# Kernel tuning notes

Hardware: AMD Instinct MI355X
Metric: run time of the kernel (lower is better)

Reference implementation:

```python
import jax, jax.numpy as jnp
import numpy as np

KERNEL_SIZE = 128
NEG_INF = -1e30


def setup_inputs() -> dict:
    key = jax.random.key(0)
    ks = jax.random.split(key, 5)
    B, S, D, H = 4, 4096, 512, 512
    x = jax.random.normal(ks[0], (B, S, D), dtype=jnp.float32)
    # torch nn.Linear weights: [out_features, in_features], y = x @ W.T + b
    Wq_w = jax.random.normal(ks[1], (H, D), dtype=jnp.float32) * (1.0 / np.sqrt(D))
    Wq_b = jax.random.normal(ks[2], (H,), dtype=jnp.float32) * 0.01
    Wk_w = jax.random.normal(ks[3], (H, D), dtype=jnp.float32) * (1.0 / np.sqrt(D))
    Wk_b = jax.random.normal(ks[4], (H,), dtype=jnp.float32) * 0.01
    return {"x": x, "Wq_w": Wq_w, "Wq_b": Wq_b, "Wk_w": Wk_w, "Wk_b": Wk_b}


def reference(x, Wq_w, Wq_b, Wk_w, Wk_b):
    # q, k: [B, S, H]
    q = jnp.einsum('bsd,hd->bsh', x, Wq_w) + Wq_b
    k = jnp.einsum('bsd,hd->bsh', x, Wk_w) + Wk_b
    # dense scores [B, S, S]
    scores = jnp.einsum('bih,bjh->bij', q, k)
    # band mask: True where i-kernel_size+1 <= j <= i+kernel_size-1
    idx = jnp.arange(x.shape[1])
    band = jnp.abs(idx[:, None] - idx[None, :]) < KERNEL_SIZE  # [S, S]
    scores = jnp.where(band[None, :, :], scores, NEG_INF)
    attn = jax.nn.softmax(scores, axis=2)
    # attend over raw x (no V projection in original module)
    return jnp.einsum('bij,bjd->bid', attn, x)
```

## Files before the change

### kernel.cpp

```cpp
#include <hip/hip_runtime.h>
#include <hip/hip_bf16.h>

#define S_LEN 4096
#define NEG_INF_F (-1e30f)

typedef __attribute__((ext_vector_type(4))) float f32x4;
typedef __attribute__((ext_vector_type(8))) short s16x8;
typedef unsigned short u16;

static __device__ __forceinline__ u16 f2bf(float f) {
    unsigned u = __builtin_bit_cast(unsigned, f);
    unsigned r = u + 0x7FFFu + ((u >> 16) & 1u);
    return (u16)(r >> 16);
}
static __device__ __forceinline__ float bf2f(u16 h) {
    unsigned u = ((unsigned)h) << 16;
    return __builtin_bit_cast(float, u);
}
static __device__ __forceinline__ void split4(const float4 v, ushort4& hi, ushort4& lo) {
    hi.x = f2bf(v.x); lo.x = f2bf(v.x - bf2f(hi.x));
    hi.y = f2bf(v.y); lo.y = f2bf(v.y - bf2f(hi.y));
    hi.z = f2bf(v.z); lo.z = f2bf(v.z - bf2f(hi.z));
    hi.w = f2bf(v.w); lo.w = f2bf(v.w - bf2f(hi.w));
}
static __device__ __forceinline__ void gl_lds16(const void* g, void* l) {
    __builtin_amdgcn_global_load_lds(
        (const __attribute__((address_space(1))) void*)g,
        (__attribute__((address_space(3))) void*)l, 16, 0, 0);
}
static __device__ __forceinline__ int swz64(int row, int col_u16) {
    return row * 64 + (col_u16 ^ ((row & 7) << 3));
}
static __device__ __forceinline__ int swz320(int row, int col_u16) {
    return row * 320 + (col_u16 ^ ((row & 7) << 3));
}
static __device__ __forceinline__ int xcd_swz512(int bid) {
    return (bid & 7) * 64 + (bid >> 3);
}

__global__ __launch_bounds__(256) void split_xt_kernel(
    const float* __restrict__ x, u16* __restrict__ xh, u16* __restrict__ xl,
    u16* __restrict__ xT) {
    const int bid = blockIdx.x;
    const int dt = bid & 7, st = (bid >> 3) & 63, b = bid >> 9;
    const int s0 = st * 64, d0 = dt * 64;
    __shared__ u16 T[64][72];
    const int tid = threadIdx.x;
    #pragma unroll
    for (int i = 0; i < 4; ++i) {
        int idx = i * 256 + tid;
        int r = idx >> 4, c4 = (idx & 15) * 4;
        float4 v = *(const float4*)(x + (size_t)(b * S_LEN + s0 + r) * 512 + d0 + c4);
        ushort4 hi, lo; split4(v, hi, lo);
        *(ushort4*)(xh + (size_t)(b * S_LEN + s0 + r) * 512 + d0 + c4) = hi;
        *(ushort4*)(xl + (size_t)(b * S_LEN + s0 + r) * 512 + d0 + c4) = lo;
        *(ushort4*)&T[r][c4] = hi;
    }
    __syncthreads();
    #pragma unroll
    for (int i = 0; i < 2; ++i) {
        int idx = i * 256 + tid;
        int dr = idx >> 3, sc = idx & 7;
        s16x8 v;
        #pragma unroll
        for (int t = 0; t < 8; ++t) v[t] = (short)T[sc * 8 + t][dr];
        *(s16x8*)&xT[(size_t)(b * 512 + d0 + dr) * S_LEN + s0 + sc * 8] = v;
    }
}

__global__ __launch_bounds__(256) void mt_kernel(
    const float* __restrict__ Wk, const float* __restrict__ Wq,
    u16* __restrict__ Mth, u16* __restrict__ Mtl) {
    const int bm = blockIdx.x & 7, bn = blockIdx.x >> 3;
    const int m0 = bm * 64, n0 = bn * 64;
    __shared__ __align__(16) u16 Ath[64 * 72], Atl[64 * 72];
    __shared__ __align__(16) u16 Bth[64 * 72], Btl[64 * 72];
    const int tid = threadIdx.x, lane = tid & 63, w = tid >> 6;
    const int frow = lane & 15, fk = (lane >> 4) * 8;
    f32x4 acc[4] = {};

    for (int h0 = 0; h0 < 512; h0 += 64) {
        #pragma unroll
        for (int i = 0; i < 4; ++i) {
            int idx = i * 256 + tid;
            int h = idx >> 4, c4 = (idx & 15) * 4;
            float4 a = *(const float4*)(Wk + (size_t)(h0 + h) * 512 + m0 + c4);
            ushort4 ahi, alo; split4(a, ahi, alo);
            Ath[(c4 + 0) * 72 + h] = ahi.x; Atl[(c4 + 0) * 72 + h] = alo.x;
            Ath[(c4 + 1) * 72 + h] = ahi.y; Atl[(c4 + 1) * 72 + h] = alo.y;
            Ath[(c4 + 2) * 72 + h] = ahi.z; Atl[(c4 + 2) * 72 + h] = alo.z;
            Ath[(c4 + 3) * 72 + h] = ahi.w; Atl[(c4 + 3) * 72 + h] = alo.w;
            float4 b = *(const float4*)(Wq + (size_t)(h0 + h) * 512 + n0 + c4);
            ushort4 bhi, blo; split4(b, bhi, blo);
            Bth[(c4 + 0) * 72 + h] = bhi.x; Btl[(c4 + 0) * 72 + h] = blo.x;
            Bth[(c4 + 1) * 72 + h] = bhi.y; Btl[(c4 + 1) * 72 + h] = blo.y;
            Bth[(c4 + 2) * 72 + h] = bhi.z; Btl[(c4 + 2) * 72 + h] = blo.z;
            Bth[(c4 + 3) * 72 + h] = bhi.w; Btl[(c4 + 3) * 72 + h] = blo.w;
        }
        __syncthreads();
        #pragma unroll
        for (int kk = 0; kk < 2; ++kk) {
            s16x8 aH = *(const s16x8*)&Ath[(w * 16 + frow) * 72 + kk * 32 + fk];
            s16x8 aL = *(const s16x8*)&Atl[(w * 16 + frow) * 72 + kk * 32 + fk];
            #pragma unroll
            for (int ni = 0; ni < 4; ++ni) {
                s16x8 bH = *(const s16x8*)&Bth[(ni * 16 + frow) * 72 + kk * 32 + fk];
                s16x8 bL = *(const s16x8*)&Btl[(ni * 16 + frow) * 72 + kk * 32 + fk];
                acc[ni] = __builtin_amdgcn_mfma_f32_16x16x32_bf16(aH, bH, acc[ni], 0, 0, 0);
                acc[ni] = __builtin_amdgcn_mfma_f32_16x16x32_bf16(aH, bL, acc[ni], 0, 0, 0);
                acc[ni] = __builtin_amdgcn_mfma_f32_16x16x32_bf16(aL, bH, acc[ni], 0, 0, 0);
            }
        }
        __syncthreads();
    }
    #pragma unroll
    for (int ni = 0; ni < 4; ++ni) {
        int d1 = n0 + ni * 16 + frow;
        #pragma unroll
        for (int e = 0; e < 4; ++e) {
            int d2 = m0 + w * 16 + (lane >> 4) * 4 + e;
            float v = acc[ni][e];
            u16 hi = f2bf(v);
            Mth[(size_t)d2 * 512 + d1] = hi;
            Mtl[(size_t)d2 * 512 + d1] = f2bf(v - bf2f(hi));
        }
    }
}

__global__ __launch_bounds__(256) void u_kernel(
    const float* __restrict__ Wk, const float* __restrict__ bq,
    float* __restrict__ u) {
    __shared__ float red[4][64];
    const int tid = threadIdx.x, c = tid & 63, hg = tid >> 6;
    const int d2 = blockIdx.x * 64 + c;
    float acc = 0.f;
    for (int h = hg; h < 512; h += 4) acc += Wk[(size_t)h * 512 + d2] * bq[h];
    red[hg][c] = acc;
    __syncthreads();
    if (hg == 0) u[d2] = red[0][c] + red[1][c] + red[2][c] + red[3][c];
}

__global__ __launch_bounds__(512) void z_kernel(
    const u16* __restrict__ xh, const u16* __restrict__ xl,
    const u16* __restrict__ Mth, const u16* __restrict__ Mtl,
    const float* __restrict__ u, u16* __restrict__ zh, u16* __restrict__ zl) {
    const int w_ = xcd_swz512((int)blockIdx.x);
    const int bm = w_ >> 2, bn = w_ & 3;
    const int m0 = bm * 128, n0 = bn * 128;
    __shared__ __align__(16) u16 Ah[128 * 64], Al[128 * 64];
    __shared__ __align__(16) u16 Bh[128 * 64], Bl[128 * 64];
    const int tid = threadIdx.x, lane = tid & 63, w = tid >> 6;
    const int rg = w >> 2, cg = w & 3;
    const int frow = lane & 15, fk = (lane >> 4) * 8;
    f32x4 acc[4][2] = {};

    for (int k0 = 0; k0 < 512; k0 += 64) {
        #pragma unroll
        for (int i = 0; i < 2; ++i) {
            int idx = i * 512 + tid;
            int r = idx >> 3, c = idx & 7;
            int sc = (c ^ (r & 7)) * 8;
            gl_lds16(xh + (size_t)(m0 + r) * 512 + k0 + sc, &Ah[idx * 8]);
            gl_lds16(xl + (size_t)(m0 + r) * 512 + k0 + sc, &Al[idx * 8]);
            gl_lds16(Mth + (size_t)(n0 + r) * 512 + k0 + sc, &Bh[idx * 8]);
            gl_lds16(Mtl + (size_t)(n0 + r) * 512 + k0 + sc, &Bl[idx * 8]);
        }
        __syncthreads();
        #pragma unroll
        for (int kk = 0; kk < 2; ++kk) {
            s16x8 aH[4], aL[4], bH[2], bL[2];
            #pragma unroll
            for (int mi = 0; mi < 4; ++mi) {
                int row = rg * 64 + mi * 16 + frow;
                aH[mi] = *(const s16x8*)&Ah[swz64(row, kk * 32 + fk)];
                aL[mi] = *(const s16x8*)&Al[swz64(row, kk * 32 + fk)];
            }
            #pragma unroll
            for (int ni = 0; ni < 2; ++ni) {
                int row = cg * 32 + ni * 16 + frow;
                bH[ni] = *(const s16x8*)&Bh[swz64(row, kk * 32 + fk)];
                bL[ni] = *(const s16x8*)&Bl[swz64(row, kk * 32 + fk)];
            }
            #pragma unroll
            for (int mi = 0; mi < 4; ++mi)
                #pragma unroll
                for (int ni = 0; ni < 2; ++ni) {
                    acc[mi][ni] = __builtin_amdgcn_mfma_f32_16x16x32_bf16(aH[mi], bH[ni], acc[mi][ni], 0, 0, 0);
                    acc[mi][ni] = __builtin_amdgcn_mfma_f32_16x16x32_bf16(aH[mi], bL[ni], acc[mi][ni], 0, 0, 0);
                    acc[mi][ni] = __builtin_amdgcn_mfma_f32_16x16x32_bf16(aL[mi], bH[ni], acc[mi][ni], 0, 0, 0);
                }
        }
        __syncthreads();
    }
    #pragma unroll
    for (int ni = 0; ni < 2; ++ni) {
        int col = n0 + cg * 32 + ni * 16 + frow;
        float uv = u[col];
        #pragma unroll
        for (int mi = 0; mi < 4; ++mi) {
            int rbase = m0 + rg * 64 + mi * 16 + (lane >> 4) * 4;
            #pragma unroll
            for (int e = 0; e < 4; ++e) {
                float v = acc[mi][ni][e] + uv;
                u16 hi = f2bf(v);
                zh[(size_t)(rbase + e) * 512 + col] = hi;
                zl[(size_t)(rbase + e) * 512 + col] = f2bf(v - bf2f(hi));
            }
        }
    }
}

__global__ __launch_bounds__(512, 4) void attn_kernel(
    const u16* __restrict__ zh, const u16* __restrict__ zl,
    const u16* __restrict__ xh, const u16* __restrict__ xl,
    const u16* __restrict__ xT, float* __restrict__ out) {
    const int w_ = xcd_swz512((int)blockIdx.x);
    const int b = w_ >> 7, it2 = w_ & 127;
    const int i0 = it2 * 32, j0 = i0 - 128;
    const int mrow0 = b * S_LEN + i0;

    __shared__ __align__(16) u16 smem[36864];
    u16* Kh = smem;
    u16* Kl = smem + 18432;
    u16* PL = smem;
    u16* VL = smem + 10240;
    __shared__ float sred_max[32 * 4], sred_sum[32 * 4];

    const int tid = threadIdx.x, lane = tid & 63, w = tid >> 6;
    const int g = w >> 2, q = w & 3;
    const int frow = lane & 15, fk = (lane >> 4) * 8;
    const int tstart = g + q * 4;
    const int nt = (q == 3) ? 5 : 4;
    const size_t qoff = (size_t)(mrow0 + g * 16 + frow) * 512;

    f32x4 acc[5] = {};

    for (int t = 0; t < 8; ++t) {
        const int k0 = t * 64;
        s16x8 aH0 = *(const s16x8*)(zh + qoff + k0 + fk);
        s16x8 aH1 = *(const s16x8*)(zh + qoff + k0 + 32 + fk);
        s16x8 aL0 = *(const s16x8*)(zl + qoff + k0 + fk);
        s16x8 aL1 = *(const s16x8*)(zl + qoff + k0 + 32 + fk);
        #pragma unroll
        for (int i = 0; i < 9; ++i) {
            int f = i * 512 + tid;
            int idx = (f < 2304) ? f : f - 2304;
            int r = idx >> 3, c = idx & 7;
            int sc = (c ^ (r & 7)) * 8;
            int j = min(max(j0 + r, 0), S_LEN - 1);
            if (f < 2304)
                gl_lds16(xh + (size_t)(b * S_LEN + j) * 512 + k0 + sc, &Kh[idx * 8]);
            else
                gl_lds16(xl + (size_t)(b * S_LEN + j) * 512 + k0 + sc, &Kl[idx * 8]);
        }
        __syncthreads();
        #pragma unroll
        for (int kk = 0; kk < 2; ++kk) {
            s16x8 aH = kk ? aH1 : aH0;
            s16x8 aL = kk ? aL1 : aL0;
            #pragma unroll
            for (int tt = 0; tt < 5; ++tt) {
                if (tt < nt) {
                    int krow = (tstart + tt) * 16 + frow;
                    s16x8 bH = *(const s16x8*)&Kh[swz64(krow, kk * 32 + fk)];
                    s16x8 bL = *(const s16x8*)&Kl[swz64(krow, kk * 32 + fk)];
                    acc[tt] = __builtin_amdgcn_mfma_f32_16x16x32_bf16(aH, bH, acc[tt], 0, 0, 0);
                    acc[tt] = __builtin_amdgcn_mfma_f32_16x16x32_bf16(aH, bL, acc[tt], 0, 0, 0);
                    acc[tt] = __builtin_amdgcn_mfma_f32_16x16x32_bf16(aL, bH, acc[tt], 0, 0, 0);
                }
            }
        }
        __syncthreads();
    }

    const int rq = (lane >> 4) * 4;
    #pragma unroll
    for (int e = 0; e < 4; ++e) {
        int r = g * 16 + rq + e;
        float m = NEG_INF_F;
        #pragma unroll
        for (int tt = 0; tt < 5; ++tt) {
            if (tt < nt) {
                int jj = (tstart + tt) * 16 + frow;
                int dj = jj - r, j = j0 + jj;
                if (dj >= 1 && dj <= 255 && j >= 0 && j < S_LEN) m = fmaxf(m, acc[tt][e]);
            }
        }
        #pragma unroll
        for (int d = 1; d < 16; d <<= 1) m = fmaxf(m, __shfl_xor(m, d));
        if (frow == 0) sred_max[r * 4 + q] = m;
    }
    __syncthreads();
    float sh[4];
    #pragma unroll
    for (int e = 0; e < 4; ++e) {
        int r = g * 16 + rq + e;
        float mx = fmaxf(fmaxf(sred_max[r * 4], sred_max[r * 4 + 1]),
                         fmaxf(sred_max[r * 4 + 2], sred_max[r * 4 + 3]));
        float s = 0.f;
        #pragma unroll
        for (int tt = 0; tt < 5; ++tt) {
            float pv = 0.f;
            if (tt < nt) {
                int jj = (tstart + tt) * 16 + frow;
                int dj = jj - r, j = j0 + jj;
                bool valid = (dj >= 1 && dj <= 255 && j >= 0 && j < S_LEN);
                pv = valid ? __expf(acc[tt][e] - mx) : 0.f;
            }
            acc[tt][e] = pv;
            s += pv;
        }
        #pragma unroll
        for (int d = 1; d < 16; d <<= 1) s += __shfl_xor(s, d);
        sh[e] = s;
    }
    if (frow == 0) {
        #pragma unroll
        for (int e = 0; e < 4; ++e) sred_sum[(g * 16 + rq + e) * 4 + q] = sh[e];
    }
    __syncthreads();
    float invv[4];
    #pragma unroll
    for (int e = 0; e < 4; ++e) {
        int r = g * 16 + rq + e;
        invv[e] = 1.f / (sred_sum[r * 4] + sred_sum[r * 4 + 1] +
                         sred_sum[r * 4 + 2] + sred_sum[r * 4 + 3]);
    }
    #pragma unroll
    for (int tt = 0; tt < 5; ++tt) {
        if (tt < nt) {
            int t = tstart + tt;
            #pragma unroll
            for (int e = 0; e < 4; ++e) {
                int r = g * 16 + rq + e;
                PL[swz320(r, t * 16 + frow)] = f2bf(acc[tt][e] * invv[e]);
            }
        }
    }
    if (q == 0) {
        int t = (g == 0) ? 17 : 0;
        int r = g * 16 + frow;
        #pragma unroll
        for (int e2 = 0; e2 < 4; ++e2)
            PL[swz320(r, t * 16 + (lane >> 4) * 4 + e2)] = 0;
    }

    for (int ds = 0; ds < 8; ++ds) {
        const int d0 = ds * 64;
        #pragma unroll
        for (int i = 0; i < 5; ++i) {
            int idx = i * 512 + tid;
            int dr = idx / 40, c8 = idx - dr * 40;
            int src = c8 ^ (dr & 7);
            int jb = j0 + src * 8;
            jb = min(max(jb, 0), S_LEN - 8);
            gl_lds16(xT + (size_t)(b * 512 + d0 + dr) * S_LEN + jb, &VL[idx * 8]);
        }
        __syncthreads();
        f32x4 po = {};
        #pragma unroll
        for (int jt = 0; jt < 9; ++jt) {
            s16x8 a = *(const s16x8*)&PL[swz320(g * 16 + frow, jt * 32 + fk)];
            s16x8 bv = *(const s16x8*)&VL[swz320(q * 16 + frow, jt * 32 + fk)];
            po = __builtin_amdgcn_mfma_f32_16x16x32_bf16(a, bv, po, 0, 0, 0);
        }
        #pragma unroll
        for (int e = 0; e < 4; ++e) {
            int r = mrow0 + g * 16 + rq + e;
            out[(size_t)r * 512 + d0 + q * 16 + frow] = po[e];
        }
        __syncthreads();
    }
}

extern "C" void kernel_launch(void* const* d_in, const int* in_sizes, int n_in,
                              void* d_out, int out_size, void* d_ws, size_t ws_size,
                              hipStream_t stream) {
    const float* x  = (const float*)d_in[0];
    const float* Wq = (const float*)d_in[1];
    const float* bq = (const float*)d_in[2];
    const float* Wk = (const float*)d_in[3];
    const float* bk = (const float*)d_in[4];
    (void)bk;
    float* out = (float*)d_out;

    u16* xh  = (u16*)d_ws;
    u16* xl  = xh + (size_t)8388608;
    u16* zh  = xl + (size_t)8388608;
    u16* zl  = zh + (size_t)8388608;
    u16* Mth = zl + (size_t)8388608;
    u16* Mtl = Mth + (size_t)262144;
    u16* xT  = Mtl + (size_t)262144;
    float* uv = (float*)(xT + (size_t)8388608);

    hipLaunchKernelGGL(split_xt_kernel, dim3(2048), dim3(256), 0, stream, x, xh, xl, xT);
    hipLaunchKernelGGL(mt_kernel, dim3(64), dim3(256), 0, stream, Wk, Wq, Mth, Mtl);
    hipLaunchKernelGGL(u_kernel, dim3(8), dim3(256), 0, stream, Wk, bq, uv);
    hipLaunchKernelGGL(z_kernel, dim3(512), dim3(512), 0, stream,
                       xh, xl, Mth, Mtl, uv, zh, zl);
    hipLaunchKernelGGL(attn_kernel, dim3(512), dim3(512), 0, stream,
                       zh, zl, xh, xl, xT, out);
}
```

Before: 141.2 us.

## Software-pipeline K and V tile loads through registers with prefetch

Replaces direct global-to-LDS async loads with register-staged prefetch: the next K/Q tile (and next V tile in the PV phase) is loaded into registers while MFMAs run on the current LDS tile, then written into swizzled LDS. It also raises wave priority around the MFMA blocks. The aim is to hide global-load latency behind compute. In exchange it adds register pressure from kreg/vreg plus extra barriers per iteration, which may lower occupancy.

```diff
diff --git a/kernel.cpp b/kernel.cpp
--- a/kernel.cpp
+++ b/kernel.cpp
@@ -235,29 +235,56 @@
 
     f32x4 acc[5] = {};
 
-    for (int t = 0; t < 8; ++t) {
+    s16x8 kreg[9];
+    auto kload = [&](int t) {
         const int k0 = t * 64;
-        s16x8 aH0 = *(const s16x8*)(zh + qoff + k0 + fk);
-        s16x8 aH1 = *(const s16x8*)(zh + qoff + k0 + 32 + fk);
-        s16x8 aL0 = *(const s16x8*)(zl + qoff + k0 + fk);
-        s16x8 aL1 = *(const s16x8*)(zl + qoff + k0 + 32 + fk);
         #pragma unroll
         for (int i = 0; i < 9; ++i) {
             int f = i * 512 + tid;
             int idx = (f < 2304) ? f : f - 2304;
             int r = idx >> 3, c = idx & 7;
-            int sc = (c ^ (r & 7)) * 8;
             int j = min(max(j0 + r, 0), S_LEN - 1);
-            if (f < 2304)
-                gl_lds16(xh + (size_t)(b * S_LEN + j) * 512 + k0 + sc, &Kh[idx * 8]);
-            else
-                gl_lds16(xl + (size_t)(b * S_LEN + j) * 512 + k0 + sc, &Kl[idx * 8]);
-        }
-        __syncthreads();
+            const u16* src = (f < 2304 ? xh : xl);
+            kreg[i] = *(const s16x8*)(src + (size_t)(b * S_LEN + j) * 512 + k0 + c * 8);
+        }
+    };
+    auto kwrite = [&]() {
+        #pragma unroll
+        for (int i = 0; i < 9; ++i) {
+            int f = i * 512 + tid;
+            int idx = (f < 2304) ? f : f - 2304;
+            int r = idx >> 3, c = idx & 7;
+            u16* dst = (f < 2304 ? Kh : Kl);
+            *(s16x8*)&dst[swz64(r, c * 8)] = kreg[i];
+        }
+    };
+
+    s16x8 zH0c, zH1c, zL0c, zL1c, zH0n, zH1n, zL0n, zL1n;
+    kload(0);
+    {
+        zH0c = *(const s16x8*)(zh + qoff + 0 + fk);
+        zH1c = *(const s16x8*)(zh + qoff + 32 + fk);
+        zL0c = *(const s16x8*)(zl + qoff + 0 + fk);
+        zL1c = *(const s16x8*)(zl + qoff + 32 + fk);
+    }
+
+    for (int t = 0; t < 8; ++t) {
+        __syncthreads();
+        kwrite();
+        __syncthreads();
+        if (t < 7) {
+            kload(t + 1);
+            const int k1 = (t + 1) * 64;
+            zH0n = *(const s16x8*)(zh + qoff + k1 + fk);
+            zH1n = *(const s16x8*)(zh + qoff + k1 + 32 + fk);
+            zL0n = *(const s16x8*)(zl + qoff + k1 + fk);
+            zL1n = *(const s16x8*)(zl + qoff + k1 + 32 + fk);
+        }
+        __builtin_amdgcn_s_setprio(1);
         #pragma unroll
         for (int kk = 0; kk < 2; ++kk) {
-            s16x8 aH = kk ? aH1 : aH0;
-            s16x8 aL = kk ? aL1 : aL0;
+            s16x8 aH = kk ? zH1c : zH0c;
+            s16x8 aL = kk ? zL1c : zL0c;
             #pragma unroll
             for (int tt = 0; tt < 5; ++tt) {
                 if (tt < nt) {
@@ -270,8 +297,31 @@
                 }
             }
         }
-        __syncthreads();
-    }
+        __builtin_amdgcn_s_setprio(0);
+        zH0c = zH0n; zH1c = zH1n; zL0c = zL0n; zL1c = zL1n;
+    }
+
+    s16x8 vreg[5];
+    auto vload = [&](int ds) {
+        const int d0 = ds * 64;
+        #pragma unroll
+        for (int i = 0; i < 5; ++i) {
+            int idx = i * 512 + tid;
+            int dr = idx / 40, c8 = idx - dr * 40;
+            int jb = j0 + c8 * 8;
+            jb = min(max(jb, 0), S_LEN - 8);
+            vreg[i] = *(const s16x8*)&xT[(size_t)(b * 512 + d0 + dr) * S_LEN + jb];
+        }
+    };
+    auto vwrite = [&]() {
+        #pragma unroll
+        for (int i = 0; i < 5; ++i) {
+            int idx = i * 512 + tid;
+            int dr = idx / 40, c8 = idx - dr * 40;
+            *(s16x8*)&VL[swz320(dr, c8 * 8)] = vreg[i];
+        }
+    };
+    vload(0);
 
     const int rq = (lane >> 4) * 4;
     #pragma unroll
@@ -346,30 +396,24 @@
     }
 
     for (int ds = 0; ds < 8; ++ds) {
-        const int d0 = ds * 64;
-        #pragma unroll
-        for (int i = 0; i < 5; ++i) {
-            int idx = i * 512 + tid;
-            int dr = idx / 40, c8 = idx - dr * 40;
-            int src = c8 ^ (dr & 7);
-            int jb = j0 + src * 8;
-            jb = min(max(jb, 0), S_LEN - 8);
-            gl_lds16(xT + (size_t)(b * 512 + d0 + dr) * S_LEN + jb, &VL[idx * 8]);
-        }
-        __syncthreads();
+        __syncthreads();
+        vwrite();
+        __syncthreads();
+        if (ds < 7) vload(ds + 1);
         f32x4 po = {};
+        __builtin_amdgcn_s_setprio(1);
         #pragma unroll
         for (int jt = 0; jt < 9; ++jt) {
             s16x8 a = *(const s16x8*)&PL[swz320(g * 16 + frow, jt * 32 + fk)];
             s16x8 bv = *(const s16x8*)&VL[swz320(q * 16 + frow, jt * 32 + fk)];
             po = __builtin_amdgcn_mfma_f32_16x16x32_bf16(a, bv, po, 0, 0, 0);
         }
+        __builtin_amdgcn_s_setprio(0);
         #pragma unroll
         for (int e = 0; e < 4; ++e) {
             int r = mrow0 + g * 16 + rq + e;
-            out[(size_t)r * 512 + d0 + q * 16 + frow] = po[e];
-        }
-        __syncthreads();
+            out[(size_t)r * 512 + ds * 64 + q * 16 + frow] = po[e];
+        }
     }
 }
 
```

Result: slower. 157.2 us (+11.3%).

## Load K and V MFMA operands directly from global memory, dropping LDS staging

Applied to the files above, without the earlier changes.

The attention kernel no longer stages key tiles and transposed-x value tiles through shared memory. Each wave now loads its MFMA B-operands straight from global memory into registers, which removes most __syncthreads barriers and shrinks LDS to just the probability tile. s_setprio is raised around the MFMA bursts. In exchange, rows shared between waves are fetched redundantly from global/L2, loads are less coalesced, and register pressure rises, which could hurt occupancy.

```diff
diff --git a/kernel.cpp b/kernel.cpp
--- a/kernel.cpp
+++ b/kernel.cpp
@@ -219,11 +219,7 @@
     const int i0 = it2 * 32, j0 = i0 - 128;
     const int mrow0 = b * S_LEN + i0;
 
-    __shared__ __align__(16) u16 smem[36864];
-    u16* Kh = smem;
-    u16* Kl = smem + 18432;
-    u16* PL = smem;
-    u16* VL = smem + 10240;
+    __shared__ __align__(16) u16 PL[32 * 320];
     __shared__ float sred_max[32 * 4], sred_sum[32 * 4];
 
     const int tid = threadIdx.x, lane = tid & 63, w = tid >> 6;
@@ -232,48 +228,50 @@
     const int tstart = g + q * 4;
     const int nt = (q == 3) ? 5 : 4;
     const size_t qoff = (size_t)(mrow0 + g * 16 + frow) * 512;
+    const int rq = (lane >> 4) * 4;
+
+    size_t rowoffs[5];
+    #pragma unroll
+    for (int tt = 0; tt < 5; ++tt) {
+        int krow = (tstart + tt) * 16 + frow;
+        int j = min(max(j0 + krow, 0), S_LEN - 1);
+        rowoffs[tt] = (size_t)(b * S_LEN + j) * 512;
+    }
 
     f32x4 acc[5] = {};
 
     for (int t = 0; t < 8; ++t) {
         const int k0 = t * 64;
-        s16x8 aH0 = *(const s16x8*)(zh + qoff + k0 + fk);
-        s16x8 aH1 = *(const s16x8*)(zh + qoff + k0 + 32 + fk);
-        s16x8 aL0 = *(const s16x8*)(zl + qoff + k0 + fk);
-        s16x8 aL1 = *(const s16x8*)(zl + qoff + k0 + 32 + fk);
-        #pragma unroll
-        for (int i = 0; i < 9; ++i) {
-            int f = i * 512 + tid;
-            int idx = (f < 2304) ? f : f - 2304;
-            int r = idx >> 3, c = idx & 7;
-            int sc = (c ^ (r & 7)) * 8;
-            int j = min(max(j0 + r, 0), S_LEN - 1);
-            if (f < 2304)
-                gl_lds16(xh + (size_t)(b * S_LEN + j) * 512 + k0 + sc, &Kh[idx * 8]);
-            else
-                gl_lds16(xl + (size_t)(b * S_LEN + j) * 512 + k0 + sc, &Kl[idx * 8]);
-        }
-        __syncthreads();
+        s16x8 zH0 = *(const s16x8*)(zh + qoff + k0 + fk);
+        s16x8 zH1 = *(const s16x8*)(zh + qoff + k0 + 32 + fk);
+        s16x8 zL0 = *(const s16x8*)(zl + qoff + k0 + fk);
+        s16x8 zL1 = *(const s16x8*)(zl + qoff + k0 + 32 + fk);
         #pragma unroll
         for (int kk = 0; kk < 2; ++kk) {
-            s16x8 aH = kk ? aH1 : aH0;
-            s16x8 aL = kk ? aL1 : aL0;
+            const int ko = k0 + kk * 32 + fk;
+            s16x8 bH[5], bL[5];
             #pragma unroll
             for (int tt = 0; tt < 5; ++tt) {
                 if (tt < nt) {
-                    int krow = (tstart + tt) * 16 + frow;
-                    s16x8 bH = *(const s16x8*)&Kh[swz64(krow, kk * 32 + fk)];
-                    s16x8 bL = *(const s16x8*)&Kl[swz64(krow, kk * 32 + fk)];
-                    acc[tt] = __builtin_amdgcn_mfma_f32_16x16x32_bf16(aH, bH, acc[tt], 0, 0, 0);
-                    acc[tt] = __builtin_amdgcn_mfma_f32_16x16x32_bf16(aH, bL, acc[tt], 0, 0, 0);
-                    acc[tt] = __builtin_amdgcn_mfma_f32_16x16x32_bf16(aL, bH, acc[tt], 0, 0, 0);
+                    bH[tt] = *(const s16x8*)(xh + rowoffs[tt] + ko);
+                    bL[tt] = *(const s16x8*)(xl + rowoffs[tt] + ko);
                 }
             }
-        }
-        __syncthreads();
-    }
-
-    const int rq = (lane >> 4) * 4;
+            s16x8 aH = kk ? zH1 : zH0;
+            s16x8 aL = kk ? zL1 : zL0;
+            __builtin_amdgcn_s_setprio(1);
+            #pragma unroll
+            for (int tt = 0; tt < 5; ++tt) {
+                if (tt < nt) {
+                    acc[tt] = __builtin_amdgcn_mfma_f32_16x16x32_bf16(aH, bH[tt], acc[tt], 0, 0, 0);
+                    acc[tt] = __builtin_amdgcn_mfma_f32_16x16x32_bf16(aH, bL[tt], acc[tt], 0, 0, 0);
+                    acc[tt] = __builtin_amdgcn_mfma_f32_16x16x32_bf16(aL, bH[tt], acc[tt], 0, 0, 0);
+                }
+            }
+            __builtin_amdgcn_s_setprio(0);
+        }
+    }
+
     #pragma unroll
     for (int e = 0; e < 4; ++e) {
         int r = g * 16 + rq + e;
@@ -344,32 +342,31 @@
         for (int e2 = 0; e2 < 4; ++e2)
             PL[swz320(r, t * 16 + (lane >> 4) * 4 + e2)] = 0;
     }
-
+    __syncthreads();
+
+    const int dvrow = q * 16 + frow;
     for (int ds = 0; ds < 8; ++ds) {
-        const int d0 = ds * 64;
-        #pragma unroll
-        for (int i = 0; i < 5; ++i) {
-            int idx = i * 512 + tid;
-            int dr = idx / 40, c8 = idx - dr * 40;
-            int src = c8 ^ (dr & 7);
-            int jb = j0 + src * 8;
+        const size_t voff = (size_t)(b * 512 + ds * 64 + dvrow) * S_LEN;
+        s16x8 bv[9];
+        #pragma unroll
+        for (int jt = 0; jt < 9; ++jt) {
+            int jb = j0 + jt * 32 + fk;
             jb = min(max(jb, 0), S_LEN - 8);
-            gl_lds16(xT + (size_t)(b * 512 + d0 + dr) * S_LEN + jb, &VL[idx * 8]);
-        }
-        __syncthreads();
+            bv[jt] = *(const s16x8*)(xT + voff + jb);
+        }
         f32x4 po = {};
+        __builtin_amdgcn_s_setprio(1);
         #pragma unroll
         for (int jt = 0; jt < 9; ++jt) {
             s16x8 a = *(const s16x8*)&PL[swz320(g * 16 + frow, jt * 32 + fk)];
-            s16x8 bv = *(const s16x8*)&VL[swz320(q * 16 + frow, jt * 32 + fk)];
-            po = __builtin_amdgcn_mfma_f32_16x16x32_bf16(a, bv, po, 0, 0, 0);
-        }
+            po = __builtin_amdgcn_mfma_f32_16x16x32_bf16(a, bv[jt], po, 0, 0, 0);
+        }
+        __builtin_amdgcn_s_setprio(0);
         #pragma unroll
         for (int e = 0; e < 4; ++e) {
             int r = mrow0 + g * 16 + rq + e;
-            out[(size_t)r * 512 + d0 + q * 16 + frow] = po[e];
-        }
-        __syncthreads();
+            out[(size_t)r * 512 + ds * 64 + q * 16 + frow] = po[e];
+        }
     }
 }
 
```

After: 205.1 us. 45.3% more time.
